# Optimization experiments

Hardware: AMD Instinct MI355X
Metric: run time of the kernel (lower is better)

Reference implementation:

```python
import jax, jax.numpy as jnp
import numpy as np

B, P, D_MODEL = 16, 256, 1024
V, D_LLM = 1000, 4096
H, DK = 16, 64  # d_keys = d_model // n_heads


def setup_inputs() -> dict:
    key = jax.random.key(0)
    ks = jax.random.split(key, 11)
    s = lambda k, shape, fan: jax.random.normal(k, shape, jnp.float32) / np.sqrt(fan)
    return {
        "target_embedding": jax.random.normal(ks[0], (B, P, D_MODEL), jnp.float32),
        "source_embedding": jax.random.normal(ks[1], (V, D_LLM), jnp.float32),
        "value_embedding": jax.random.normal(ks[2], (V, D_LLM), jnp.float32),
        "Wq": s(ks[3], (D_MODEL, H * DK), D_MODEL),
        "bq": jnp.zeros((H * DK,), jnp.float32),
        "Wk": s(ks[4], (D_LLM, H * DK), D_LLM),
        "bk": jnp.zeros((H * DK,), jnp.float32),
        "Wv": s(ks[5], (D_LLM, H * DK), D_LLM),
        "bv": jnp.zeros((H * DK,), jnp.float32),
        "Wo": s(ks[6], (H * DK, D_LLM), H * DK),
        "bo": jnp.zeros((D_LLM,), jnp.float32),
    }


def reference(target_embedding, source_embedding, value_embedding,
              Wq, bq, Wk, bk, Wv, bv, Wo, bo):
    b, p, _ = target_embedding.shape
    v = source_embedding.shape[0]
    # projections
    Q = (target_embedding @ Wq + bq).reshape(b, p, H, DK)   # bphd
    K = (source_embedding @ Wk + bk).reshape(v, H, DK)      # vhd
    Vv = (value_embedding @ Wv + bv).reshape(v, H, DK)      # vhd
    scale = 1.0 / np.sqrt(DK)
    # NOTE: non-standard einsum — contracts over v, elementwise in d
    scores = jnp.einsum('bphd,vhd->bhpd', Q, K)             # [B,H,P,DK]
    A = jax.nn.softmax(scale * scores, axis=-1)             # softmax over head dim d
    # (dropout is identity in eval mode)
    R = jnp.einsum('bhpd,vhd->bphd', A, Vv)                 # A * sum_v V
    out = R.reshape(b, p, H * DK) @ Wo + bo                 # [B,P,D_LLM]
    return out
```

## Files before the change

### kernel.cpp

```cpp
#include <hip/hip_runtime.h>

#define BB   16
#define PP   256
#define BP   4096
#define DMODEL 1024
#define VV   1000
#define DLLM 4096
#define HH   16
#define DK   64
#define HDK  1024

using f32x4 = __attribute__((ext_vector_type(4))) float;
using s16x8 = __attribute__((ext_vector_type(8))) short;

__device__ __forceinline__ unsigned short f2bf(float f) {
    unsigned int u = __builtin_bit_cast(unsigned int, f);
    u = (u + 0x7FFFu + ((u >> 16) & 1u)) >> 16;
    return (unsigned short)u;
}

__device__ __forceinline__ void gload_lds16(const unsigned short* g, unsigned short* lds) {
    __builtin_amdgcn_global_load_lds(
        (const __attribute__((address_space(1))) void*)g,
        (__attribute__((address_space(3))) void*)lds,
        16, 0, 0);
}

__device__ __forceinline__ void transpose_body(const float* __restrict__ src,
                                               unsigned short* __restrict__ dst,
                                               int R, int C, int bx, int by, int t,
                                               float (*tile)[33]) {
    int tx = t & 31, ty = t >> 5;
    int c0 = bx * 32, r0 = by * 32;
#pragma unroll
    for (int j = 0; j < 4; ++j)
        tile[ty + j * 8][tx] = src[(size_t)(r0 + ty + j * 8) * C + c0 + tx];
    __syncthreads();
#pragma unroll
    for (int j = 0; j < 4; ++j)
        dst[(size_t)(c0 + ty + j * 8) * R + r0 + tx] = f2bf(tile[tx][ty + j * 8]);
}

__global__ void mega1(const float* __restrict__ src0, const float* __restrict__ src1,
                      float* __restrict__ part1,
                      const float* __restrict__ target, unsigned short* __restrict__ tgt_bf,
                      const float* __restrict__ Wq, unsigned short* __restrict__ wq_t,
                      const float* __restrict__ Wo, unsigned short* __restrict__ wo_t) {
    __shared__ float tile[32][33];
    int b = blockIdx.x, t = threadIdx.x;
    if (b < 1280) {
        int x = b & 15, y = (b >> 4) % 40, z = b / 640;
        int col = x * 256 + t;
        const float* src = z ? src1 : src0;
        int r0 = y * 25;
        float acc = 0.f;
        for (int r = 0; r < 25; ++r)
            acc += src[(size_t)(r0 + r) * DLLM + col];
        part1[((z * 40 + y) * DLLM) + col] = acc;
    } else if (b < 1280 + 4096) {
        int idx = (b - 1280) * 256 + t;
        float4 v = reinterpret_cast<const float4*>(target)[idx];
        ushort4 o = make_ushort4(f2bf(v.x), f2bf(v.y), f2bf(v.z), f2bf(v.w));
        reinterpret_cast<ushort4*>(tgt_bf)[idx] = o;
    } else if (b < 1280 + 4096 + 1024) {
        int b2 = b - 5376;
        transpose_body(Wq, wq_t, DMODEL, HDK, b2 & 31, b2 >> 5, t, tile);
    } else {
        int b2 = b - 6400;
        transpose_body(Wo, wo_t, HDK, DLLM, b2 & 127, b2 >> 7, t, tile);
    }
}

__global__ void gemv_partial2(const float* __restrict__ Wk, const float* __restrict__ Wv,
                              const float* __restrict__ part1, float* __restrict__ part2) {
    __shared__ float vec[64];
    int c     = blockIdx.x * 256 + threadIdx.x;
    int chunk = blockIdx.y;
    int z     = blockIdx.z;
    const float* W = z ? Wv : Wk;
    if (threadIdx.x < 64) {
        int r = chunk * 64 + threadIdx.x;
        float a = 0.f;
        for (int p = 0; p < 40; ++p)
            a += part1[(size_t)(z * 40 + p) * DLLM + r];
        vec[threadIdx.x] = a;
    }
    __syncthreads();
    float acc = 0.f;
    int r0 = chunk * 64;
    for (int r = 0; r < 64; ++r)
        acc += vec[r] * W[(size_t)(r0 + r) * HDK + c];
    part2[((z * 64 + chunk) * HDK) + c] = acc;
}

__global__ void gemv_reduce(const float* __restrict__ part,
                            const float* __restrict__ bk, const float* __restrict__ bv,
                            float* __restrict__ kvsum) {
    int idx = blockIdx.x * 256 + threadIdx.x;
    int z = idx >> 10, c = idx & 1023;
    float acc = 0.f;
    for (int ch = 0; ch < 64; ++ch) acc += part[(size_t)(z * 64 + ch) * HDK + c];
    acc += (float)VV * (z ? bv[c] : bk[c]);
    kvsum[idx] = acc;
}

template<int EPI, int BMt, int BNt, int WM, int WN>
__global__ __launch_bounds__(WM * WN * 64, 2)
void gemm_ctd3(const unsigned short* __restrict__ A, const unsigned short* __restrict__ Bt,
               float* __restrict__ C, const float* __restrict__ bias,
               const float* __restrict__ kvsum, unsigned short* __restrict__ R,
               int N, int K, int gx) {
    constexpr int WAVES = WM * WN;
    constexpr int Mw = BMt / WM;
    constexpr int M_REP = Mw / 16;
    constexpr int NA = BMt * 32 / (WAVES * 512);
    constexpr int NB = BNt * 32 / (WAVES * 512);
    constexpr int NST = NA + NB;
    static_assert(BNt / WN == 64, "wave col span must be 64");
    static_assert(NA >= 1 && NB >= 1, "staging geometry");

    __shared__ __align__(16) unsigned short Asm[3][BMt * 32];
    __shared__ __align__(16) unsigned short Bsm[3][BNt * 32];

    const int nwg = gridDim.x, q8 = nwg >> 3;
    const int nb = (blockIdx.x & 7) * q8 + (blockIdx.x >> 3);
    const int bm = (nb / gx) * BMt;
    const int bn = (nb % gx) * BNt;

    const int t = threadIdx.x;
    const int w = t >> 6, lane = t & 63;
    const int wr = w / WN, wc = w % WN;
    const int l15 = lane & 15, kgrp = lane >> 4;

    size_t goffA[NA], goffB[NB];
    int ldsoA[NA], ldsoB[NB];
    {
        int s8 = lane & 7, jj = lane >> 3;
#pragma unroll
        for (int i = 0; i < NA; ++i) {
            int sr = (i * WAVES + w) * 8 + jj;
            int x = s8 ^ (sr & 7);
            goffA[i] = (size_t)(bm + sr * 2 + (x >> 2)) * K + (x & 3) * 8;
            ldsoA[i] = (i * WAVES + w) * 512;
        }
#pragma unroll
        for (int i = 0; i < NB; ++i) {
            int sr = (i * WAVES + w) * 8 + jj;
            int x = s8 ^ (sr & 7);
            goffB[i] = (size_t)(bn + sr * 2 + (x >> 2)) * K + (x & 3) * 8;
            ldsoB[i] = (i * WAVES + w) * 512;
        }
    }
    int ra[M_REP], rb[4];
#pragma unroll
    for (int m = 0; m < M_REP; ++m) {
        int r = wr * Mw + m * 16 + l15;
        int s8 = (kgrp + 4 * (r & 1)) ^ ((r >> 1) & 7);
        ra[m] = (r >> 1) * 64 + s8 * 8;
    }
#pragma unroll
    for (int n = 0; n < 4; ++n) {
        int r = wc * 64 + n * 16 + l15;
        int s8 = (kgrp + 4 * (r & 1)) ^ ((r >> 1) & 7);
        rb[n] = (r >> 1) * 64 + s8 * 8;
    }

    f32x4 acc[M_REP][4] = {};

#define STAGE(t_, b_) do { size_t k0_ = (size_t)(t_) * 32;             \
    _Pragma("unroll")                                                  \
    for (int i_ = 0; i_ < NA; ++i_)                                    \
        gload_lds16(A + goffA[i_] + k0_, &Asm[b_][ldsoA[i_]]);         \
    _Pragma("unroll")                                                  \
    for (int i_ = 0; i_ < NB; ++i_)                                    \
        gload_lds16(Bt + goffB[i_] + k0_, &Bsm[b_][ldsoB[i_]]); } while (0)

#define WAIT_VM(n_) asm volatile("s_waitcnt vmcnt(" #n_ ")" ::: "memory")

    const int nT = K >> 5;
    STAGE(0, 0); STAGE(1, 1);
    if constexpr (NST == 6) WAIT_VM(6); else if constexpr (NST == 4) WAIT_VM(4); else WAIT_VM(3);
    __builtin_amdgcn_s_barrier();

    int cur = 0;
    for (int tk = 0; tk < nT; ++tk) {
        s16x8 af[M_REP], bfr[4];
#pragma unroll
        for (int m = 0; m < M_REP; ++m)
            af[m] = *reinterpret_cast<const s16x8*>(&Asm[cur][ra[m]]);
#pragma unroll
        for (int n = 0; n < 4; ++n)
            bfr[n] = *reinterpret_cast<const s16x8*>(&Bsm[cur][rb[n]]);
        if (tk + 2 < nT) STAGE(tk + 2, cur == 0 ? 2 : cur - 1);
        __builtin_amdgcn_s_setprio(1);
#pragma unroll
        for (int m = 0; m < M_REP; ++m)
#pragma unroll
            for (int n = 0; n < 4; ++n)
                acc[m][n] = __builtin_amdgcn_mfma_f32_16x16x32_bf16(af[m], bfr[n], acc[m][n], 0, 0, 0);
        __builtin_amdgcn_s_setprio(0);
        if (tk + 2 < nT) {
            if constexpr (NST == 6) WAIT_VM(6); else if constexpr (NST == 4) WAIT_VM(4); else WAIT_VM(3);
        } else if (tk + 1 < nT) {
            WAIT_VM(0);
        }
        if (tk + 1 < nT) __builtin_amdgcn_s_barrier();
        cur = (cur == 2) ? 0 : cur + 1;
    }
#undef STAGE
#undef WAIT_VM

    if (EPI == 0) {
#pragma unroll
        for (int m = 0; m < M_REP; ++m) {
            int grow = bm + wr * Mw + m * 16 + kgrp * 4;
#pragma unroll
            for (int n = 0; n < 4; ++n) {
                int gcol = bn + wc * 64 + n * 16 + l15;
                float bb = bias[gcol];
#pragma unroll
                for (int j = 0; j < 4; ++j)
                    C[(size_t)(grow + j) * N + gcol] = acc[m][n][j] + bb;
            }
        }
    } else {
        float bqv[4], ksv[4], vsv[4];
#pragma unroll
        for (int n = 0; n < 4; ++n) {
            int col = bn + wc * 64 + n * 16 + l15;
            bqv[n] = bias[col];
            ksv[n] = kvsum[col];
            vsv[n] = kvsum[HDK + col];
        }
#pragma unroll
        for (int m = 0; m < M_REP; ++m) {
            int grow = bm + wr * Mw + m * 16 + kgrp * 4;
#pragma unroll
            for (int j = 0; j < 4; ++j) {
                float x[4];
#pragma unroll
                for (int n = 0; n < 4; ++n)
                    x[n] = 0.125f * (acc[m][n][j] + bqv[n]) * ksv[n];
                float mx = fmaxf(fmaxf(x[0], x[1]), fmaxf(x[2], x[3]));
#pragma unroll
                for (int off = 8; off; off >>= 1) mx = fmaxf(mx, __shfl_xor(mx, off));
                float e[4], s = 0.f;
#pragma unroll
                for (int n = 0; n < 4; ++n) { e[n] = __expf(x[n] - mx); s += e[n]; }
#pragma unroll
                for (int off = 8; off; off >>= 1) s += __shfl_xor(s, off);
                float inv = 1.0f / s;
#pragma unroll
                for (int n = 0; n < 4; ++n) {
                    int col = bn + wc * 64 + n * 16 + l15;
                    R[(size_t)(grow + j) * N + col] = f2bf(e[n] * inv * vsv[n]);
                }
            }
        }
    }
}

extern "C" void kernel_launch(void* const* d_in, const int* in_sizes, int n_in,
                              void* d_out, int out_size, void* d_ws, size_t ws_size,
                              hipStream_t stream) {
    const float* target = (const float*)d_in[0];
    const float* source = (const float*)d_in[1];
    const float* value  = (const float*)d_in[2];
    const float* Wq = (const float*)d_in[3];
    const float* bq = (const float*)d_in[4];
    const float* Wk = (const float*)d_in[5];
    const float* bk = (const float*)d_in[6];
    const float* Wv = (const float*)d_in[7];
    const float* bv = (const float*)d_in[8];
    const float* Wo = (const float*)d_in[9];
    const float* bo = (const float*)d_in[10];
    float* out = (float*)d_out;

    char* ws = (char*)d_ws;
    float*          part1  = (float*)(ws);
    float*          part2  = (float*)(ws + 0x180000);
    float*          kvsum  = (float*)(ws + 0x210000);
    unsigned short* tgt_bf = (unsigned short*)(ws + 0x400000);
    unsigned short* wq_t   = (unsigned short*)(ws + 0xC00000);
    unsigned short* wo_t   = (unsigned short*)(ws + 0xE00000);
    unsigned short* Rb     = (unsigned short*)(ws + 0x1600000);

    mega1<<<10496, 256, 0, stream>>>(source, value, part1, target, tgt_bf, Wq, wq_t, Wo, wo_t);

    gemv_partial2<<<dim3(4, 64, 2), 256, 0, stream>>>(Wk, Wv, part1, part2);
    gemv_reduce<<<8, 256, 0, stream>>>(part2, bk, bv, kvsum);

    gemm_ctd3<1, 128, 64, 4, 1><<<512, 256, 0, stream>>>(
        tgt_bf, wq_t, nullptr, bq, kvsum, Rb, HDK, DMODEL, HDK / 64);

    gemm_ctd3<0, 256, 128, 2, 2><<<512, 256, 0, stream>>>(
        Rb, wo_t, out, bo, nullptr, nullptr, DLLM, HDK, DLLM / 128);
}
```

Before: 92.54 us.

## Vectorize prep kernel loads, remap GEMM tiles per XCD, retile Q GEMM

The prep kernel now uses float4 loads for the column-sum and the transposes, and 8-wide bf16 stores for the target conversion, which cuts the block count. Both GEMMs replace the generic block swizzle with an explicit XCD-aware mapping that gives each XCD an 8x8 tile neighbourhood, aiming for better L2 reuse. The Q GEMM changes to a 64x128 tile with two waves per block. The output GEMM writes with nontemporal stores to avoid polluting the cache. The new tile mapping depends on exact grid sizes, and the 2-wave blocks may lower occupancy or latency hiding.

```diff
diff --git a/kernel.cpp b/kernel.cpp
--- a/kernel.cpp
+++ b/kernel.cpp
@@ -12,6 +12,7 @@
 
 using f32x4 = __attribute__((ext_vector_type(4))) float;
 using s16x8 = __attribute__((ext_vector_type(8))) short;
+using us8   = __attribute__((ext_vector_type(8))) unsigned short;
 
 __device__ __forceinline__ unsigned short f2bf(float f) {
     unsigned int u = __builtin_bit_cast(unsigned int, f);
@@ -30,15 +31,15 @@
                                                unsigned short* __restrict__ dst,
                                                int R, int C, int bx, int by, int t,
                                                float (*tile)[33]) {
-    int tx = t & 31, ty = t >> 5;
+    int x = t & 7, y = t >> 3;
     int c0 = bx * 32, r0 = by * 32;
-#pragma unroll
-    for (int j = 0; j < 4; ++j)
-        tile[ty + j * 8][tx] = src[(size_t)(r0 + ty + j * 8) * C + c0 + tx];
+    float4 v = *reinterpret_cast<const float4*>(&src[(size_t)(r0 + y) * C + c0 + x * 4]);
+    tile[y][x * 4 + 0] = v.x; tile[y][x * 4 + 1] = v.y;
+    tile[y][x * 4 + 2] = v.z; tile[y][x * 4 + 3] = v.w;
     __syncthreads();
-#pragma unroll
-    for (int j = 0; j < 4; ++j)
-        dst[(size_t)(c0 + ty + j * 8) * R + r0 + tx] = f2bf(tile[tx][ty + j * 8]);
+    ushort4 o = make_ushort4(f2bf(tile[x * 4 + 0][y]), f2bf(tile[x * 4 + 1][y]),
+                             f2bf(tile[x * 4 + 2][y]), f2bf(tile[x * 4 + 3][y]));
+    *reinterpret_cast<ushort4*>(&dst[(size_t)(c0 + y) * R + r0 + x * 4]) = o;
 }
 
 __global__ void mega1(const float* __restrict__ src0, const float* __restrict__ src1,
@@ -48,25 +49,29 @@
                       const float* __restrict__ Wo, unsigned short* __restrict__ wo_t) {
     __shared__ float tile[32][33];
     int b = blockIdx.x, t = threadIdx.x;
-    if (b < 1280) {
-        int x = b & 15, y = (b >> 4) % 40, z = b / 640;
-        int col = x * 256 + t;
-        const float* src = z ? src1 : src0;
+    if (b < 320) {
+        int z = b / 160, rem = b % 160, y = rem >> 2, x = rem & 3;
+        int col4 = x * 256 + t;
+        const float4* src = reinterpret_cast<const float4*>(z ? src1 : src0);
         int r0 = y * 25;
-        float acc = 0.f;
-        for (int r = 0; r < 25; ++r)
-            acc += src[(size_t)(r0 + r) * DLLM + col];
-        part1[((z * 40 + y) * DLLM) + col] = acc;
-    } else if (b < 1280 + 4096) {
-        int idx = (b - 1280) * 256 + t;
-        float4 v = reinterpret_cast<const float4*>(target)[idx];
-        ushort4 o = make_ushort4(f2bf(v.x), f2bf(v.y), f2bf(v.z), f2bf(v.w));
-        reinterpret_cast<ushort4*>(tgt_bf)[idx] = o;
-    } else if (b < 1280 + 4096 + 1024) {
-        int b2 = b - 5376;
+        float4 acc = make_float4(0.f, 0.f, 0.f, 0.f);
+        for (int r = 0; r < 25; ++r) {
+            float4 v = src[(size_t)(r0 + r) * (DLLM / 4) + col4];
+            acc.x += v.x; acc.y += v.y; acc.z += v.z; acc.w += v.w;
+        }
+        reinterpret_cast<float4*>(part1)[(size_t)(z * 40 + y) * (DLLM / 4) + col4] = acc;
+    } else if (b < 320 + 2048) {
+        int idx = (b - 320) * 256 + t;
+        float4 v0 = reinterpret_cast<const float4*>(target)[idx * 2];
+        float4 v1 = reinterpret_cast<const float4*>(target)[idx * 2 + 1];
+        us8 o = { f2bf(v0.x), f2bf(v0.y), f2bf(v0.z), f2bf(v0.w),
+                  f2bf(v1.x), f2bf(v1.y), f2bf(v1.z), f2bf(v1.w) };
+        *reinterpret_cast<us8*>(&tgt_bf[(size_t)idx * 8]) = o;
+    } else if (b < 320 + 2048 + 1024) {
+        int b2 = b - 2368;
         transpose_body(Wq, wq_t, DMODEL, HDK, b2 & 31, b2 >> 5, t, tile);
     } else {
-        int b2 = b - 6400;
+        int b2 = b - 3392;
         transpose_body(Wo, wo_t, HDK, DLLM, b2 & 127, b2 >> 7, t, tile);
     }
 }
@@ -109,7 +114,7 @@
 void gemm_ctd3(const unsigned short* __restrict__ A, const unsigned short* __restrict__ Bt,
                float* __restrict__ C, const float* __restrict__ bias,
                const float* __restrict__ kvsum, unsigned short* __restrict__ R,
-               int N, int K, int gx) {
+               int N, int K, int gDivR) {
     constexpr int WAVES = WM * WN;
     constexpr int Mw = BMt / WM;
     constexpr int M_REP = Mw / 16;
@@ -122,10 +127,9 @@
     __shared__ __align__(16) unsigned short Asm[3][BMt * 32];
     __shared__ __align__(16) unsigned short Bsm[3][BNt * 32];
 
-    const int nwg = gridDim.x, q8 = nwg >> 3;
-    const int nb = (blockIdx.x & 7) * q8 + (blockIdx.x >> 3);
-    const int bm = (nb / gx) * BMt;
-    const int bn = (nb % gx) * BNt;
+    const int xcd = blockIdx.x & 7, l = blockIdx.x >> 3;
+    const int bm = ((xcd / gDivR) * 8 + (l & 7)) * BMt;
+    const int bn = ((xcd % gDivR) * 8 + (l >> 3)) * BNt;
 
     const int t = threadIdx.x;
     const int w = t >> 6, lane = t & 63;
@@ -220,7 +224,8 @@
                 float bb = bias[gcol];
 #pragma unroll
                 for (int j = 0; j < 4; ++j)
-                    C[(size_t)(grow + j) * N + gcol] = acc[m][n][j] + bb;
+                    __builtin_nontemporal_store(acc[m][n][j] + bb,
+                                                &C[(size_t)(grow + j) * N + gcol]);
             }
         }
     } else {
@@ -285,14 +290,14 @@
     unsigned short* wo_t   = (unsigned short*)(ws + 0xE00000);
     unsigned short* Rb     = (unsigned short*)(ws + 0x1600000);
 
-    mega1<<<10496, 256, 0, stream>>>(source, value, part1, target, tgt_bf, Wq, wq_t, Wo, wo_t);
+    mega1<<<7488, 256, 0, stream>>>(source, value, part1, target, tgt_bf, Wq, wq_t, Wo, wo_t);
 
     gemv_partial2<<<dim3(4, 64, 2), 256, 0, stream>>>(Wk, Wv, part1, part2);
     gemv_reduce<<<8, 256, 0, stream>>>(part2, bk, bv, kvsum);
 
-    gemm_ctd3<1, 128, 64, 4, 1><<<512, 256, 0, stream>>>(
-        tgt_bf, wq_t, nullptr, bq, kvsum, Rb, HDK, DMODEL, HDK / 64);
+    gemm_ctd3<1, 64, 128, 1, 2><<<512, 128, 0, stream>>>(
+        tgt_bf, wq_t, nullptr, bq, kvsum, Rb, HDK, DMODEL, 1);
 
     gemm_ctd3<0, 256, 128, 2, 2><<<512, 256, 0, stream>>>(
-        Rb, wo_t, out, bo, nullptr, nullptr, DLLM, HDK, DLLM / 128);
-}
+        Rb, wo_t, out, bo, nullptr, nullptr, DLLM, HDK, 4);
+}
```

Measured after the change: 109.4 us (median of 2 runs). 18.2% more time.
